# Kernel tuning notes

Measured on AMD Instinct MI355X. Metric: run time of the kernel, lower is better.

## Reference

```python
import jax, jax.numpy as jnp
import numpy as np

EPS = 1e-9
C, Hd, Wd = 3, 64, 64  # input_dimensions[1:]

def setup_inputs() -> dict:
    key = jax.random.key(0)
    ks = jax.random.split(key, 8)
    S, B = 8, 512
    num_digits, num_style, num_hidden, bott, num_pixels = 10, 50, 512, 160, C * Hd * Wd
    return {
        "digits": jax.random.uniform(ks[0], (S, B, num_digits), dtype=jnp.float32),
        "styles": jax.random.normal(ks[1], (S, B, num_style), dtype=jnp.float32),
        "images": jax.random.uniform(ks[2], (S, B, C, Hd, Wd), dtype=jnp.float32),
        "W_h": jax.random.normal(ks[3], (num_digits + num_style, num_hidden), dtype=jnp.float32) * 0.05,
        "b_h": jnp.zeros((num_hidden,), jnp.float32),
        "W1": jax.random.normal(ks[4], (num_hidden, bott), dtype=jnp.float32) * 0.05,
        "b1": jnp.zeros((bott,), jnp.float32),
        "W2": jax.random.normal(ks[5], (bott, num_pixels), dtype=jnp.float32) * 0.05,
        "b2": jnp.zeros((num_pixels,), jnp.float32),
    }

def reference(digits, styles, images, W_h, b_h, W1, b1, W2, b2):
    # dec_hidden: Linear + ReLU, fully batched over [S, B]
    h = jax.nn.relu(jnp.concatenate([digits, styles], axis=-1) @ W_h + b_h)  # [S,B,Hn]
    # hidden_pass (original loops per-sample; here a single batched GEMM chain)
    t = jax.nn.selu(h @ W1 + b1)                 # [S,B,160]
    x_hat = jax.nn.sigmoid(t @ W2 + b2)          # [S,B,P]
    S, B, _ = x_hat.shape
    images_mean = x_hat.reshape(S, B, C, Hd, Wd)
    # eps-guarded BCE-style log-likelihood loss, summed over last dim only
    loss = -(jnp.log(images_mean + EPS) * images
             + jnp.log(1.0 - images_mean + EPS) * (1.0 - images)).sum(-1)  # [S,B,C,Hd]
    return loss
```

## Files before the change

### kernel.cpp

```cpp
#include <hip/hip_runtime.h>
#include <hip/hip_bf16.h>
#include <math.h>


#define SELU_SCALE 1.0507009873554804934193349852946f
#define SELU_ALPHA 1.6732632423543772848170429916717f

typedef __attribute__((ext_vector_type(8))) short bf16x8;
typedef __attribute__((ext_vector_type(4))) float f32x4;

static __device__ __forceinline__ short f2bf(float x) {
    __hip_bfloat16 h = __float2bfloat16(x);
    short s;
    __builtin_memcpy(&s, &h, 2);
    return s;
}

__global__ __launch_bounds__(256) void w2_pack_kernel(
    const float* __restrict__ W2,
    __hip_bfloat16* __restrict__ w2f)
{
    __shared__ float tile[32][64];
    const int colBase = blockIdx.x * 64;
    const int kkBase  = blockIdx.y * 32;
    const int tid = threadIdx.x;

    for (int i = tid; i < 32 * 64; i += 256)
        tile[i >> 6][i & 63] = W2[(size_t)(kkBase + (i >> 6)) * 12288 + colBase + (i & 63)];
    __syncthreads();

    const int c16 = tid >> 6;
    const int lane = tid & 63;
    const int lr = lane & 15, lh = lane >> 4;

    bf16x8 v;
#pragma unroll
    for (int j = 0; j < 8; ++j)
        v[j] = f2bf(tile[lh * 8 + j][c16 * 16 + lr]);

    const size_t chunk = (size_t)(blockIdx.x * 4 + c16) * 5 + blockIdx.y;
    *(bf16x8*)((short*)w2f + chunk * 512 + lane * 8) = v;
}

__global__ __launch_bounds__(512) void dec_fused_kernel(
    const float* __restrict__ digits,
    const float* __restrict__ styles,
    const float* __restrict__ Wh,
    const float* __restrict__ bh,
    const float* __restrict__ W1,
    const float* __restrict__ b1,
    __hip_bfloat16* __restrict__ tf)
{
    __shared__ float cat_s[16][60];
    __shared__ float h_s[16 * 512];
    __shared__ float t_s[16][161];

    const int tid = threadIdx.x;
    const int rowBase = blockIdx.x * 16;

    for (int i = tid; i < 16 * 60; i += 512) {
        const int r = i / 60, k = i % 60;
        const int row = rowBase + r;
        cat_s[r][k] = (k < 10) ? digits[row * 10 + k]
                               : styles[row * 50 + (k - 10)];
    }
    __syncthreads();

    {
        float acc[16];
        const float bias = bh[tid];
#pragma unroll
        for (int r = 0; r < 16; ++r) acc[r] = bias;
        for (int k = 0; k < 60; ++k) {
            const float w = Wh[k * 512 + tid];
#pragma unroll
            for (int r = 0; r < 16; ++r) acc[r] = fmaf(cat_s[r][k], w, acc[r]);
        }
#pragma unroll
        for (int r = 0; r < 16; ++r)
            h_s[r * 512 + tid] = fmaxf(acc[r], 0.0f);
    }
    __syncthreads();

    if (tid < 320) {
        const int rh = (tid >= 160) ? 1 : 0;
        const int col = tid - rh * 160;
        const int r0 = rh * 8;
        float acc[8];
        const float bias = b1[col];
#pragma unroll
        for (int r = 0; r < 8; ++r) acc[r] = bias;

        for (int k = 0; k < 512; k += 4) {
            const float w0 = W1[(size_t)(k + 0) * 160 + col];
            const float w1 = W1[(size_t)(k + 1) * 160 + col];
            const float w2 = W1[(size_t)(k + 2) * 160 + col];
            const float w3 = W1[(size_t)(k + 3) * 160 + col];
#pragma unroll
            for (int r = 0; r < 8; ++r) {
                const float4 hv = *(const float4*)&h_s[(r0 + r) * 512 + k];
                float a = acc[r];
                a = fmaf(hv.x, w0, a);
                a = fmaf(hv.y, w1, a);
                a = fmaf(hv.z, w2, a);
                a = fmaf(hv.w, w3, a);
                acc[r] = a;
            }
        }
#pragma unroll
        for (int r = 0; r < 8; ++r) {
            const float z = acc[r];
            const float s = (z > 0.0f) ? (SELU_SCALE * z)
                                       : (SELU_SCALE * SELU_ALPHA * expm1f(z));
            t_s[r0 + r][col] = s;
        }
    }
    __syncthreads();

    if (tid < 320) {
        const int kk = tid >> 6;
        const int l = tid & 63;
        const int lr = l & 15, lh = l >> 4;
        bf16x8 v;
#pragma unroll
        for (int j = 0; j < 8; ++j)
            v[j] = f2bf(t_s[lr][kk * 32 + lh * 8 + j]);
        *(bf16x8*)((short*)tf + ((size_t)blockIdx.x * 5 + kk) * 512 + l * 8) = v;
    }
}

__global__ __launch_bounds__(256, 5) void out_loss_mfma_kernel(
    const __hip_bfloat16* __restrict__ tf,
    const __hip_bfloat16* __restrict__ w2f,
    const float* __restrict__ b2,
    const float* __restrict__ images,
    float* __restrict__ out)
{
    __shared__ float ims[4][2048];

    const int tid = threadIdx.x;
    const int lane = tid & 63;
    const int wv = tid >> 6;
    const int rowBase = blockIdx.y * 128 + wv * 32;
    const int colBase = blockIdx.x * 64;
    const int lr = lane & 15;
    const int lh = lane >> 4;

    const short* wfb = (const short*)w2f;
    const short* tfb = (const short*)tf;
    const char* imb = (const char*)images;

    {
        const int rsub = lane >> 4;
        const int m = lane & 15;
#pragma unroll
        for (int w = 0; w < 8; ++w) {
            const int r = w * 4 + rsub;
            const size_t gb = (size_t)(rowBase + r) * 49152 + (size_t)colBase * 4
                            + (size_t)((16 * m) ^ ((r & 15) << 4));
            __builtin_amdgcn_global_load_lds((const uint32_t*)(imb + gb),
                (uint32_t*)&ims[wv][w * 256], 16, 0, 0);
        }
    }

    const int c16base = blockIdx.x * 4;
    const int r16base = rowBase >> 4;

    f32x4 acc[4][2] = {};
#pragma unroll
    for (int kk = 0; kk < 5; ++kk) {
        bf16x8 bT[2], aW[4];
#pragma unroll
        for (int r = 0; r < 2; ++r)
            bT[r] = *(const bf16x8*)(tfb
                + ((size_t)(r16base + r) * 5 + kk) * 512 + lane * 8);
#pragma unroll
        for (int c = 0; c < 4; ++c)
            aW[c] = *(const bf16x8*)(wfb
                + ((size_t)(c16base + c) * 5 + kk) * 512 + lane * 8);
#pragma unroll
        for (int c = 0; c < 4; ++c)
#pragma unroll
            for (int r = 0; r < 2; ++r)
                acc[c][r] = __builtin_amdgcn_mfma_f32_16x16x32_bf16(
                    aW[c], bT[r], acc[c][r], 0, 0, 0);
    }

    float4 bc[4];
#pragma unroll
    for (int c = 0; c < 4; ++c)
        bc[c] = *(const float4*)(b2 + colBase + c * 16 + lh * 4);

    asm volatile("s_waitcnt vmcnt(0)" ::: "memory");
    __builtin_amdgcn_sched_barrier(0);

    const float* myq = ims[wv];
#pragma unroll
    for (int rw = 0; rw < 2; ++rw) {
        float mx = 0.f;
        float pr = 1.f;
        float zi = 0.f;
#pragma unroll
        for (int c = 0; c < 4; ++c) {
            const int fidx = (rw * 16 + lr) * 64 + ((lh * 4 + c * 16) ^ (lr << 2));
            const float4 im4 = *(const float4*)&myq[fidx];
            const float imv[4] = {im4.x, im4.y, im4.z, im4.w};
            const float bcv[4] = {bc[c].x, bc[c].y, bc[c].z, bc[c].w};
#pragma unroll
            for (int j = 0; j < 4; ++j) {
                const float z = acc[c][rw][j] + bcv[j];
                mx += fmaxf(z, 0.0f);
                pr *= 1.0f + __expf(-fabsf(z));
                zi = fmaf(z, imv[j], zi);
            }
        }
        float part = mx + __logf(pr) - zi;

        part += __shfl_xor(part, 16);
        part += __shfl_xor(part, 32);

        if (lane < 16)
            out[(size_t)(rowBase + rw * 16 + lane) * 192 + blockIdx.x] = part;
    }
}

extern "C" void kernel_launch(void* const* d_in, const int* in_sizes, int n_in,
                              void* d_out, int out_size, void* d_ws, size_t ws_size,
                              hipStream_t stream) {
    const float* digits = (const float*)d_in[0];
    const float* styles = (const float*)d_in[1];
    const float* images = (const float*)d_in[2];
    const float* Wh     = (const float*)d_in[3];
    const float* bh     = (const float*)d_in[4];
    const float* W1     = (const float*)d_in[5];
    const float* b1     = (const float*)d_in[6];
    const float* W2     = (const float*)d_in[7];
    const float* b2     = (const float*)d_in[8];
    float* out = (float*)d_out;

    __hip_bfloat16* w2f = (__hip_bfloat16*)d_ws;
    __hip_bfloat16* tf  = w2f + (size_t)12288 * 160;

    dim3 gridP(192, 5);
    w2_pack_kernel<<<gridP, 256, 0, stream>>>(W2, w2f);

    dec_fused_kernel<<<256, 512, 0, stream>>>(digits, styles, Wh, bh, W1, b1, tf);

    dim3 grid3(192, 32);
    out_loss_mfma_kernel<<<grid3, 256, 0, stream>>>(tf, w2f, b2, images, out);
}
```

Baseline: 91.46 us.

## Loop over four column tiles per wave with double-buffered image prefetch

The output/loss kernel now gives each wave 16 rows across four 64-column tiles, not 32 rows of one tile. The t fragments are loaded once into registers and reused across the tiles. Image slabs are double-buffered in LDS through global_load_lds, so the next tile's images load while the current tile runs its MFMA and loss math. This cuts the block count and the repeated t loads, and overlaps the image streaming with compute, at the cost of a serial per-block loop and the tuning of the vmcnt wait counts.

```diff
diff --git a/kernel.cpp b/kernel.cpp
--- a/kernel.cpp
+++ b/kernel.cpp
@@ -136,79 +136,91 @@
     const float* __restrict__ images,
     float* __restrict__ out)
 {
-    __shared__ float ims[4][2048];
+    __shared__ float ims[4][2][1024];
 
     const int tid = threadIdx.x;
     const int lane = tid & 63;
     const int wv = tid >> 6;
-    const int rowBase = blockIdx.y * 128 + wv * 32;
-    const int colBase = blockIdx.x * 64;
+    const int rowBase = blockIdx.y * 64 + wv * 16;
+    const int colBase0 = blockIdx.x * 256;
     const int lr = lane & 15;
     const int lh = lane >> 4;
 
     const short* wfb = (const short*)w2f;
     const short* tfb = (const short*)tf;
     const char* imb = (const char*)images;
-
-    {
-        const int rsub = lane >> 4;
-        const int m = lane & 15;
-#pragma unroll
-        for (int w = 0; w < 8; ++w) {
-            const int r = w * 4 + rsub;
-            const size_t gb = (size_t)(rowBase + r) * 49152 + (size_t)colBase * 4
-                            + (size_t)((16 * m) ^ ((r & 15) << 4));
-            __builtin_amdgcn_global_load_lds((const uint32_t*)(imb + gb),
-                (uint32_t*)&ims[wv][w * 256], 16, 0, 0);
-        }
-    }
-
-    const int c16base = blockIdx.x * 4;
-    const int r16base = rowBase >> 4;
-
-    f32x4 acc[4][2] = {};
-#pragma unroll
-    for (int kk = 0; kk < 5; ++kk) {
-        bf16x8 bT[2], aW[4];
-#pragma unroll
-        for (int r = 0; r < 2; ++r)
-            bT[r] = *(const bf16x8*)(tfb
-                + ((size_t)(r16base + r) * 5 + kk) * 512 + lane * 8);
+    const int r16 = rowBase >> 4;
+
+    const int rsub = lane >> 4;
+    const int m16 = lane & 15;
+
+    bf16x8 bT[5];
+#pragma unroll
+    for (int kk = 0; kk < 5; ++kk)
+        bT[kk] = *(const bf16x8*)(tfb + ((size_t)r16 * 5 + kk) * 512 + lane * 8);
+
+#pragma unroll
+    for (int w = 0; w < 4; ++w) {
+        const int r = w * 4 + rsub;
+        const size_t gb = (size_t)(rowBase + r) * 49152 + (size_t)colBase0 * 4
+                        + (size_t)((16 * m16) ^ ((r & 15) << 4));
+        __builtin_amdgcn_global_load_lds((const uint32_t*)(imb + gb),
+            (uint32_t*)&ims[wv][0][w * 256], 16, 0, 0);
+    }
+
+#pragma unroll
+    for (int it = 0; it < 4; ++it) {
+        const int colB = colBase0 + it * 64;
+        const int c16b = colB >> 4;
+
+        f32x4 acc[4] = {};
+#pragma unroll
+        for (int kk = 0; kk < 5; ++kk) {
+            bf16x8 aW[4];
+#pragma unroll
+            for (int c = 0; c < 4; ++c)
+                aW[c] = *(const bf16x8*)(wfb
+                    + ((size_t)(c16b + c) * 5 + kk) * 512 + lane * 8);
+#pragma unroll
+            for (int c = 0; c < 4; ++c)
+                acc[c] = __builtin_amdgcn_mfma_f32_16x16x32_bf16(
+                    aW[c], bT[kk], acc[c], 0, 0, 0);
+        }
+
+        float4 bc[4];
 #pragma unroll
         for (int c = 0; c < 4; ++c)
-            aW[c] = *(const bf16x8*)(wfb
-                + ((size_t)(c16base + c) * 5 + kk) * 512 + lane * 8);
-#pragma unroll
-        for (int c = 0; c < 4; ++c)
-#pragma unroll
-            for (int r = 0; r < 2; ++r)
-                acc[c][r] = __builtin_amdgcn_mfma_f32_16x16x32_bf16(
-                    aW[c], bT[r], acc[c][r], 0, 0, 0);
-    }
-
-    float4 bc[4];
-#pragma unroll
-    for (int c = 0; c < 4; ++c)
-        bc[c] = *(const float4*)(b2 + colBase + c * 16 + lh * 4);
-
-    asm volatile("s_waitcnt vmcnt(0)" ::: "memory");
-    __builtin_amdgcn_sched_barrier(0);
-
-    const float* myq = ims[wv];
-#pragma unroll
-    for (int rw = 0; rw < 2; ++rw) {
+            bc[c] = *(const float4*)(b2 + colB + c * 16 + lh * 4);
+
+        if (it < 3) {
+            const int colN = colBase0 + (it + 1) * 64;
+#pragma unroll
+            for (int w = 0; w < 4; ++w) {
+                const int r = w * 4 + rsub;
+                const size_t gb = (size_t)(rowBase + r) * 49152
+                                + (size_t)colN * 4
+                                + (size_t)((16 * m16) ^ ((r & 15) << 4));
+                __builtin_amdgcn_global_load_lds((const uint32_t*)(imb + gb),
+                    (uint32_t*)&ims[wv][(it + 1) & 1][w * 256], 16, 0, 0);
+            }
+            asm volatile("s_waitcnt vmcnt(4)" ::: "memory");
+        } else {
+            asm volatile("s_waitcnt vmcnt(0)" ::: "memory");
+        }
+
+        const float* slab = ims[wv][it & 1];
         float mx = 0.f;
         float pr = 1.f;
         float zi = 0.f;
 #pragma unroll
         for (int c = 0; c < 4; ++c) {
-            const int fidx = (rw * 16 + lr) * 64 + ((lh * 4 + c * 16) ^ (lr << 2));
-            const float4 im4 = *(const float4*)&myq[fidx];
+            const int fidx = lr * 64 + ((lh * 4 + c * 16) ^ (lr << 2));
+            const float4 im4 = *(const float4*)&slab[fidx];
             const float imv[4] = {im4.x, im4.y, im4.z, im4.w};
             const float bcv[4] = {bc[c].x, bc[c].y, bc[c].z, bc[c].w};
 #pragma unroll
             for (int j = 0; j < 4; ++j) {
-                const float z = acc[c][rw][j] + bcv[j];
+                const float z = acc[c][j] + bcv[j];
                 mx += fmaxf(z, 0.0f);
                 pr *= 1.0f + __expf(-fabsf(z));
                 zi = fmaf(z, imv[j], zi);
@@ -220,7 +232,7 @@
         part += __shfl_xor(part, 32);
 
         if (lane < 16)
-            out[(size_t)(rowBase + rw * 16 + lane) * 192 + blockIdx.x] = part;
+            out[(size_t)(rowBase + lane) * 192 + blockIdx.x * 4 + it] = part;
     }
 }
 
@@ -246,6 +258,6 @@
 
     dec_fused_kernel<<<256, 512, 0, stream>>>(digits, styles, Wh, bh, W1, b1, tf);
 
-    dim3 grid3(192, 32);
+    dim3 grid3(48, 64);
     out_loss_mfma_kernel<<<grid3, 256, 0, stream>>>(tf, w2f, b2, images, out);
 }
```

After: 122.1 us. 33.5% more time.
